# Performance work log

Measured on AMD Instinct MI355X. Metric: run time of the kernel, lower is better.

## Reference

```python
import jax, jax.numpy as jnp
import numpy as np

B, C, H, W = 16, 64, 64, 64
O, BR, K = 128, 3, 3  # out_channels, branch, kernel


def setup_inputs() -> dict:
    key = jax.random.key(0)
    k1, k2, k3, k4 = jax.random.split(key, 4)
    x = jax.random.normal(k1, (B, C, H, W), dtype=jnp.float32)
    w1 = jax.random.normal(k2, (O, BR * BR), dtype=jnp.float32) * 0.1
    w2 = jax.random.normal(k3, (O, BR), dtype=jnp.float32) * 0.1
    conn = jax.random.randint(k4, (O * BR * BR,), 0, C * K * K)
    return {"x": x, "w1": w1, "w2": w2, "conn": conn}


def reference(x, w1, w2, conn):
    # replicate pad (kernel 3x3, extra_pad=0 -> pad 1 on each side)
    x_pad = jnp.pad(x, ((0, 0), (0, 0), (1, 1), (1, 1)), mode='edge')
    # extract 3x3 patches, stride 1; loop is over fixed 9 kernel offsets
    # patches: [B, C, H, W, K*K] with (i,j) row-major, matching torch unfold
    patches = jnp.stack(
        [x_pad[:, :, i:i + H, j:j + W] for i in range(K) for j in range(K)],
        axis=-1,
    )
    # -> [B, H, W, C*K*K]   (flatten order C, k0, k1 as in the torch reshape)
    patches = jnp.transpose(patches, (0, 2, 3, 1, 4)).reshape(B, H, W, C * K * K)
    # random gather along the unfolded axis -> [B, H, W, O, BR*BR]
    g = patches[..., conn].reshape(B, H, W, O, BR * BR)
    g = jnp.transpose(g, (0, 3, 1, 2, 4))  # [B, O, H, W, BR*BR]
    d = jnp.abs(g - w1[:, None, None, :])  # broadcast w1 [O,1,1,BR*BR]
    ma = jnp.max(d.reshape(B, O, H, W, BR, BR), axis=-1)  # amax over inner branch
    mi = jnp.min(jnp.abs(ma - w2[:, None, None, :]), axis=-1)  # amin over branch
    return mi  # [B, O, H, W]
```

## Files before the change

### kernel.cpp

```cpp
#include <hip/hip_runtime.h>

#define BB 16
#define CC 64
#define HH 64
#define WW 64
#define OO 128
#define HALO 6
#define SLAB_DW (CC * HALO * WW)
#define LDS_BYTES (SLAB_DW * 4)

extern "C" __global__ __launch_bounds__(1024, 1) void minimax_conv_kernel(
    const float* __restrict__ x, const float* __restrict__ w1,
    const float* __restrict__ w2, const int* __restrict__ conn,
    float* __restrict__ out)
{
    extern __shared__ float xs[];

    const int tid = threadIdx.x;
    const int bid = blockIdx.x;
    const int b  = bid >> 4;
    const int r0 = (bid & 15) * 4;

    const float* xb = x + (size_t)b * (CC * HH * WW);

    float4 tmp[6];
    #pragma unroll
    for (int rnd = 0; rnd < 6; ++rnd) {
        const int f   = rnd * 1024 + tid;
        const int c   = f / 96;
        const int rem = f * 4 - c * (HALO * WW);
        const int rl  = rem >> 6;
        const int col = rem & 63;
        int rimg = r0 - 1 + rl;
        rimg = rimg < 0 ? 0 : (rimg > HH - 1 ? HH - 1 : rimg);
        tmp[rnd] = *(const float4*)(xb + (c * HH + rimg) * WW + col);
    }
    #pragma unroll
    for (int rnd = 0; rnd < 6; ++rnd) {
        const int f = rnd * 1024 + tid;
        *(float4*)(xs + f * 4) = tmp[rnd];
    }
    __syncthreads();

    const int lane = tid & 63;
    const int Wv   = __builtin_amdgcn_readfirstlane(tid >> 6);
    const int colm = (lane == 0)  ? 0  : lane - 1;
    const int colp = (lane == 63) ? 63 : lane + 1;

    #pragma unroll 2
    for (int tt = 0; tt < 16; ++tt) {
        const int task = Wv + 16 * tt;
        const int o  = task & 127;
        const int pp = task >> 7;

        float rA, rB;
        #pragma unroll
        for (int p = 0; p < 3; ++p) {
            float eA, eB;
            #pragma unroll
            for (int q = 0; q < 3; ++q) {
                const int t = p * 3 + q;
                const int v = conn[o * 9 + t];
                const int c = v / 9;
                const int r9 = v - c * 9;
                const int i = r9 / 3;
                const int j = r9 - i * 3;
                const float w1v = w1[o * 9 + t];

                const int col = (j == 0) ? colm : ((j == 1) ? lane : colp);
                const float* pb = xs + c * (HALO * WW) + (2 * pp + i) * WW + col;
                const float gA = pb[0];
                const float gB = pb[WW];
                const float dA = fabsf(gA - w1v);
                const float dB = fabsf(gB - w1v);
                if (q == 0) { eA = dA; eB = dB; }
                else        { eA = fmaxf(eA, dA); eB = fmaxf(eB, dB); }
            }
            const float w2v = w2[o * 3 + p];
            const float mA = fabsf(eA - w2v);
            const float mB = fabsf(eB - w2v);
            if (p == 0) { rA = mA; rB = mB; }
            else        { rA = fminf(rA, mA); rB = fminf(rB, mB); }
        }

        float* ob = out + (((size_t)b * OO + o) * HH + (r0 + 2 * pp)) * WW + lane;
        ob[0]  = rA;
        ob[WW] = rB;
    }
}

extern "C" void kernel_launch(void* const* d_in, const int* in_sizes, int n_in,
                              void* d_out, int out_size, void* d_ws, size_t ws_size,
                              hipStream_t stream) {
    const float* x    = (const float*)d_in[0];
    const float* w1   = (const float*)d_in[1];
    const float* w2   = (const float*)d_in[2];
    const int*   conn = (const int*)d_in[3];
    float* out = (float*)d_out;

    hipFuncSetAttribute((const void*)minimax_conv_kernel,
                        hipFuncAttributeMaxDynamicSharedMemorySize, LDS_BYTES);

    const int blocks = BB * 16;
    minimax_conv_kernel<<<blocks, 1024, LDS_BYTES, stream>>>(x, w1, w2, conn, out);
}
```

Baseline: 36.81 us.

## Use smaller 2-row blocks of 512 threads for higher occupancy and nontemporal stores

Each block now covers 2 output rows instead of 4, with 512 threads instead of 1024. That shrinks the LDS slab from 6 halo rows to 4 per channel (64KB) and doubles the grid to 512 blocks, so several blocks can be resident per CU and the tail is better balanced. Each wave now handles 16 output channels for the block's row pair. Output writes use nontemporal stores to avoid polluting the cache. The cost is more redundant halo loading, since each block reloads 4 rows to produce 2.

```diff
diff --git a/kernel.cpp b/kernel.cpp
--- a/kernel.cpp
+++ b/kernel.cpp
@@ -5,11 +5,11 @@
 #define HH 64
 #define WW 64
 #define OO 128
-#define HALO 6
-#define SLAB_DW (CC * HALO * WW)
+#define ROWS 4
+#define SLAB_DW (CC * ROWS * WW)
 #define LDS_BYTES (SLAB_DW * 4)
 
-extern "C" __global__ __launch_bounds__(1024, 1) void minimax_conv_kernel(
+extern "C" __global__ __launch_bounds__(512, 4) void minimax_conv_kernel(
     const float* __restrict__ x, const float* __restrict__ w1,
     const float* __restrict__ w2, const int* __restrict__ conn,
     float* __restrict__ out)
@@ -18,40 +18,35 @@
 
     const int tid = threadIdx.x;
     const int bid = blockIdx.x;
-    const int b  = bid >> 4;
-    const int r0 = (bid & 15) * 4;
+    const int b  = bid >> 5;
+    const int r0 = (bid & 31) * 2;
 
     const float* xb = x + (size_t)b * (CC * HH * WW);
 
-    float4 tmp[6];
     #pragma unroll
-    for (int rnd = 0; rnd < 6; ++rnd) {
-        const int f   = rnd * 1024 + tid;
-        const int c   = f / 96;
-        const int rem = f * 4 - c * (HALO * WW);
-        const int rl  = rem >> 6;
-        const int col = rem & 63;
+    for (int rnd = 0; rnd < 8; ++rnd) {
+        const int f    = rnd * 512 + tid;
+        const int c    = f >> 6;
+        const int rem  = f & 63;
+        const int rl   = rem >> 4;
+        const int colq = (rem & 15) * 4;
         int rimg = r0 - 1 + rl;
         rimg = rimg < 0 ? 0 : (rimg > HH - 1 ? HH - 1 : rimg);
-        tmp[rnd] = *(const float4*)(xb + (c * HH + rimg) * WW + col);
-    }
-    #pragma unroll
-    for (int rnd = 0; rnd < 6; ++rnd) {
-        const int f = rnd * 1024 + tid;
-        *(float4*)(xs + f * 4) = tmp[rnd];
+        const float4 v = *(const float4*)(xb + (c * HH + rimg) * WW + colq);
+        *(float4*)(xs + f * 4) = v;
     }
     __syncthreads();
 
     const int lane = tid & 63;
-    const int Wv   = __builtin_amdgcn_readfirstlane(tid >> 6);
+    const int wv   = __builtin_amdgcn_readfirstlane(tid >> 6);
     const int colm = (lane == 0)  ? 0  : lane - 1;
     const int colp = (lane == 63) ? 63 : lane + 1;
 
-    #pragma unroll 2
-    for (int tt = 0; tt < 16; ++tt) {
-        const int task = Wv + 16 * tt;
-        const int o  = task & 127;
-        const int pp = task >> 7;
+    float* outb = out + (((size_t)b * OO) * HH + r0) * WW + lane;
+
+    #pragma unroll 4
+    for (int oi = 0; oi < 16; ++oi) {
+        const int o = wv * 16 + oi;
 
         float rA, rB;
         #pragma unroll
@@ -68,7 +63,7 @@
                 const float w1v = w1[o * 9 + t];
 
                 const int col = (j == 0) ? colm : ((j == 1) ? lane : colp);
-                const float* pb = xs + c * (HALO * WW) + (2 * pp + i) * WW + col;
+                const float* pb = xs + c * (ROWS * WW) + i * WW + col;
                 const float gA = pb[0];
                 const float gB = pb[WW];
                 const float dA = fabsf(gA - w1v);
@@ -83,9 +78,9 @@
             else        { rA = fminf(rA, mA); rB = fminf(rB, mB); }
         }
 
-        float* ob = out + (((size_t)b * OO + o) * HH + (r0 + 2 * pp)) * WW + lane;
-        ob[0]  = rA;
-        ob[WW] = rB;
+        float* ob = outb + (size_t)o * (HH * WW);
+        __builtin_nontemporal_store(rA, ob);
+        __builtin_nontemporal_store(rB, ob + WW);
     }
 }
 
@@ -101,6 +96,6 @@
     hipFuncSetAttribute((const void*)minimax_conv_kernel,
                         hipFuncAttributeMaxDynamicSharedMemorySize, LDS_BYTES);
 
-    const int blocks = BB * 16;
-    minimax_conv_kernel<<<blocks, 1024, LDS_BYTES, stream>>>(x, w1, w2, conn, out);
+    const int blocks = BB * 32;
+    minimax_conv_kernel<<<blocks, 512, LDS_BYTES, stream>>>(x, w1, w2, conn, out);
 }
```

New measurement: 32.45 us. 11.9% less time.
